# Optimization experiments

Hardware: AMD Instinct MI355X
Metric: run time of the kernel (lower is better)

## Reference

```python
import jax, jax.numpy as jnp
import numpy as np

N_ITERS = 21
TEMPERATURE = 0.04


def setup_inputs() -> dict:
    key = jax.random.key(0)
    input_tensor = jax.random.normal(key, (4096, 128, 128), dtype=jnp.float32)
    return {"input_tensor": input_tensor}


def reference(input_tensor) -> jnp.ndarray:
    n = input_tensor.shape[1]
    log_alpha = input_tensor.reshape((-1, n, n)) / TEMPERATURE

    def body(_, la):
        la = la - jax.nn.logsumexp(la, axis=2, keepdims=True)  # row normalize
        la = la - jax.nn.logsumexp(la, axis=1, keepdims=True)  # col normalize
        return la

    log_alpha = jax.lax.fori_loop(0, N_ITERS, body, log_alpha)
    return jnp.exp(log_alpha)
```

## Files before the change

### kernel.cpp

```cpp
#include <hip/hip_runtime.h>

typedef short bf16x8 __attribute__((ext_vector_type(8)));
typedef float f32x4 __attribute__((ext_vector_type(4)));
typedef unsigned int u32;
typedef unsigned short u16;

#define NIT 21
#define SMIN 1e-33f
#define LDSCOL 136

static __device__ __forceinline__ u16 f2bf(float f) {
    u32 u = __float_as_uint(f);
    u = (u + 0x7fffu + ((u >> 16) & 1u)) >> 16;
    return (u16)u;
}
static __device__ __forceinline__ float bf2f(u16 h) {
    return __uint_as_float(((u32)h) << 16);
}

__global__ __launch_bounds__(512)
void sinkhorn_kernel(const float* __restrict__ in, float* __restrict__ out) {
    const int t  = threadIdx.x;
    const int w  = t >> 6;
    const int lg = (t >> 4) & 3;
    const int ln = t & 15;
    const int M  = w * 16 + ln;
    const size_t mat = (size_t)blockIdx.x << 14;
    const float S = 36.067376022224085f;

    __shared__ __align__(16) u16 Ecm[128 * LDSCOL];
    __shared__ __align__(16) u16 a_lds[128];
    __shared__ __align__(16) u16 b_lds[128];

    bf16x8 af[4];

    {
        const float* src = in + mat + (size_t)M * 128 + lg * 8;
        float v[4][8];
        float m = -3.4e38f;
#pragma unroll
        for (int c = 0; c < 4; ++c) {
            float4 f0 = *(const float4*)(src + c * 32);
            float4 f1 = *(const float4*)(src + c * 32 + 4);
            v[c][0] = f0.x; v[c][1] = f0.y; v[c][2] = f0.z; v[c][3] = f0.w;
            v[c][4] = f1.x; v[c][5] = f1.y; v[c][6] = f1.z; v[c][7] = f1.w;
#pragma unroll
            for (int j = 0; j < 8; ++j) m = fmaxf(m, v[c][j]);
        }
        m = fmaxf(m, __shfl_xor(m, 16));
        m = fmaxf(m, __shfl_xor(m, 32));
        const float nms = -m * S;
        float s = 0.f;
#pragma unroll
        for (int c = 0; c < 4; ++c) {
            bf16x8 fr;
#pragma unroll
            for (int j = 0; j < 8; ++j) {
                float e = __builtin_amdgcn_exp2f(fmaf(v[c][j], S, nms));
                s += e;
                fr[j] = (short)f2bf(e);
            }
            af[c] = fr;
#pragma unroll
            for (int j = 0; j < 8; ++j)
                Ecm[(c * 32 + lg * 8 + j) * LDSCOL + M] = (u16)fr[j];
        }
        s += __shfl_xor(s, 16);
        s += __shfl_xor(s, 32);
        if (lg == 0) a_lds[M] = f2bf(__builtin_amdgcn_rcpf(fmaxf(s, SMIN)));
    }
    __syncthreads();

    const f32x4 z4 = {0.f, 0.f, 0.f, 0.f};

#pragma unroll 1
    for (int it = 0; it < NIT; ++it) {
        f32x4 acc = z4;
#pragma unroll
        for (int c = 0; c < 4; ++c) {
            const int kb = c * 32 + lg * 8;
            bf16x8 aop = *(const bf16x8*)&a_lds[kb];
            bf16x8 bop = *(const bf16x8*)&Ecm[M * LDSCOL + kb];
            acc = __builtin_amdgcn_mfma_f32_16x16x32_bf16(aop, bop, acc, 0, 0, 0);
        }
        if (lg == 0)
            b_lds[M] = f2bf(__builtin_amdgcn_rcpf(fmaxf(acc[0], SMIN)));
        __syncthreads();

        if (it < NIT - 1) {
            f32x4 r0 = z4;
#pragma unroll
            for (int c = 0; c < 4; ++c) {
                bf16x8 bop = *(const bf16x8*)&b_lds[c * 32 + lg * 8];
                r0 = __builtin_amdgcn_mfma_f32_16x16x32_bf16(af[c], bop, r0, 0, 0, 0);
            }
            if (ln == 0) {
#pragma unroll
                for (int r = 0; r < 4; ++r)
                    a_lds[w * 16 + lg * 4 + r] =
                        f2bf(__builtin_amdgcn_rcpf(fmaxf(r0[r], SMIN)));
            }
            __syncthreads();
        }
    }

    {
        float* dst = out + mat + (size_t)M * 128 + lg * 8;
        const float av = bf2f(a_lds[M]);
#pragma unroll
        for (int c = 0; c < 4; ++c) {
            const bf16x8 e = af[c];
            const bf16x8 bop = *(const bf16x8*)&b_lds[c * 32 + lg * 8];
            float4 o0, o1;
            o0.x = bf2f((u16)e[0]) * av * bf2f((u16)bop[0]);
            o0.y = bf2f((u16)e[1]) * av * bf2f((u16)bop[1]);
            o0.z = bf2f((u16)e[2]) * av * bf2f((u16)bop[2]);
            o0.w = bf2f((u16)e[3]) * av * bf2f((u16)bop[3]);
            o1.x = bf2f((u16)e[4]) * av * bf2f((u16)bop[4]);
            o1.y = bf2f((u16)e[5]) * av * bf2f((u16)bop[5]);
            o1.z = bf2f((u16)e[6]) * av * bf2f((u16)bop[6]);
            o1.w = bf2f((u16)e[7]) * av * bf2f((u16)bop[7]);
            *(float4*)(dst + c * 32)     = o0;
            *(float4*)(dst + c * 32 + 4) = o1;
        }
    }
}

extern "C" void kernel_launch(void* const* d_in, const int* in_sizes, int n_in,
                              void* d_out, int out_size, void* d_ws, size_t ws_size,
                              hipStream_t stream) {
    (void)n_in; (void)d_ws; (void)ws_size; (void)out_size;
    const float* in  = (const float*)d_in[0];
    float*       out = (float*)d_out;
    const int n_mat = in_sizes[0] / (128 * 128);
    sinkhorn_kernel<<<dim3(n_mat), dim3(512), 0, stream>>>(in, out);
}
```

Before: 150.5 us.

## Process two matrices per block to interleave independent MFMA chains

Each 512-thread block now handles two matrices instead of one, keeping two sets of LDS scaling vectors and exponent tiles and interleaving their MFMA chains within each Sinkhorn iteration. This halves the number of barriers per matrix and gives the scheduler independent MFMA work to hide latency in the serial row/column normalization loop. In exchange LDS use per block doubles (about 70 KB), which lowers occupancy, register pressure rises from holding two fragment sets, and the grid shrinks by half. An odd matrix count would leave the last matrix unprocessed.

```diff
diff --git a/kernel.cpp b/kernel.cpp
--- a/kernel.cpp
+++ b/kernel.cpp
@@ -25,17 +25,18 @@
     const int lg = (t >> 4) & 3;
     const int ln = t & 15;
     const int M  = w * 16 + ln;
-    const size_t mat = (size_t)blockIdx.x << 14;
+    const size_t mat0 = (size_t)(2 * blockIdx.x) << 14;
     const float S = 36.067376022224085f;
 
-    __shared__ __align__(16) u16 Ecm[128 * LDSCOL];
-    __shared__ __align__(16) u16 a_lds[128];
-    __shared__ __align__(16) u16 b_lds[128];
+    __shared__ __align__(16) u16 Ecm[2][128 * LDSCOL];
+    __shared__ __align__(16) u16 a_lds[2][128];
+    __shared__ __align__(16) u16 b_lds[2][128];
 
-    bf16x8 af[4];
+    bf16x8 af[2][4];
 
-    {
-        const float* src = in + mat + (size_t)M * 128 + lg * 8;
+#pragma unroll
+    for (int pm = 0; pm < 2; ++pm) {
+        const float* src = in + mat0 + ((size_t)pm << 14) + (size_t)M * 128 + lg * 8;
         float v[4][8];
         float m = -3.4e38f;
 #pragma unroll
@@ -60,14 +61,14 @@
                 s += e;
                 fr[j] = (short)f2bf(e);
             }
-            af[c] = fr;
+            af[pm][c] = fr;
 #pragma unroll
             for (int j = 0; j < 8; ++j)
-                Ecm[(c * 32 + lg * 8 + j) * LDSCOL + M] = (u16)fr[j];
+                Ecm[pm][(c * 32 + lg * 8 + j) * LDSCOL + M] = (u16)fr[j];
         }
         s += __shfl_xor(s, 16);
         s += __shfl_xor(s, 32);
-        if (lg == 0) a_lds[M] = f2bf(__builtin_amdgcn_rcpf(fmaxf(s, SMIN)));
+        if (lg == 0) a_lds[pm][M] = f2bf(__builtin_amdgcn_rcpf(fmaxf(s, SMIN)));
     }
     __syncthreads();
 
@@ -75,42 +76,54 @@
 
 #pragma unroll 1
     for (int it = 0; it < NIT; ++it) {
-        f32x4 acc = z4;
+        f32x4 acc0 = z4, acc1 = z4;
 #pragma unroll
         for (int c = 0; c < 4; ++c) {
             const int kb = c * 32 + lg * 8;
-            bf16x8 aop = *(const bf16x8*)&a_lds[kb];
-            bf16x8 bop = *(const bf16x8*)&Ecm[M * LDSCOL + kb];
-            acc = __builtin_amdgcn_mfma_f32_16x16x32_bf16(aop, bop, acc, 0, 0, 0);
+            bf16x8 a0 = *(const bf16x8*)&a_lds[0][kb];
+            bf16x8 e0 = *(const bf16x8*)&Ecm[0][M * LDSCOL + kb];
+            bf16x8 a1 = *(const bf16x8*)&a_lds[1][kb];
+            bf16x8 e1 = *(const bf16x8*)&Ecm[1][M * LDSCOL + kb];
+            acc0 = __builtin_amdgcn_mfma_f32_16x16x32_bf16(a0, e0, acc0, 0, 0, 0);
+            acc1 = __builtin_amdgcn_mfma_f32_16x16x32_bf16(a1, e1, acc1, 0, 0, 0);
         }
-        if (lg == 0)
-            b_lds[M] = f2bf(__builtin_amdgcn_rcpf(fmaxf(acc[0], SMIN)));
+        if (lg == 0) {
+            b_lds[0][M] = f2bf(__builtin_amdgcn_rcpf(fmaxf(acc0[0], SMIN)));
+            b_lds[1][M] = f2bf(__builtin_amdgcn_rcpf(fmaxf(acc1[0], SMIN)));
+        }
         __syncthreads();
 
         if (it < NIT - 1) {
-            f32x4 r0 = z4;
+            f32x4 r0 = z4, r1 = z4;
 #pragma unroll
             for (int c = 0; c < 4; ++c) {
-                bf16x8 bop = *(const bf16x8*)&b_lds[c * 32 + lg * 8];
-                r0 = __builtin_amdgcn_mfma_f32_16x16x32_bf16(af[c], bop, r0, 0, 0, 0);
+                const int kb = c * 32 + lg * 8;
+                bf16x8 b0 = *(const bf16x8*)&b_lds[0][kb];
+                bf16x8 b1 = *(const bf16x8*)&b_lds[1][kb];
+                r0 = __builtin_amdgcn_mfma_f32_16x16x32_bf16(af[0][c], b0, r0, 0, 0, 0);
+                r1 = __builtin_amdgcn_mfma_f32_16x16x32_bf16(af[1][c], b1, r1, 0, 0, 0);
             }
             if (ln == 0) {
 #pragma unroll
-                for (int r = 0; r < 4; ++r)
-                    a_lds[w * 16 + lg * 4 + r] =
+                for (int r = 0; r < 4; ++r) {
+                    a_lds[0][w * 16 + lg * 4 + r] =
                         f2bf(__builtin_amdgcn_rcpf(fmaxf(r0[r], SMIN)));
+                    a_lds[1][w * 16 + lg * 4 + r] =
+                        f2bf(__builtin_amdgcn_rcpf(fmaxf(r1[r], SMIN)));
+                }
             }
             __syncthreads();
         }
     }
 
-    {
-        float* dst = out + mat + (size_t)M * 128 + lg * 8;
-        const float av = bf2f(a_lds[M]);
+#pragma unroll
+    for (int pm = 0; pm < 2; ++pm) {
+        float* dst = out + mat0 + ((size_t)pm << 14) + (size_t)M * 128 + lg * 8;
+        const float av = bf2f(a_lds[pm][M]);
 #pragma unroll
         for (int c = 0; c < 4; ++c) {
-            const bf16x8 e = af[c];
-            const bf16x8 bop = *(const bf16x8*)&b_lds[c * 32 + lg * 8];
+            const bf16x8 e = af[pm][c];
+            const bf16x8 bop = *(const bf16x8*)&b_lds[pm][c * 32 + lg * 8];
             float4 o0, o1;
             o0.x = bf2f((u16)e[0]) * av * bf2f((u16)bop[0]);
             o0.y = bf2f((u16)e[1]) * av * bf2f((u16)bop[1]);
@@ -133,5 +146,5 @@
     const float* in  = (const float*)d_in[0];
     float*       out = (float*)d_out;
     const int n_mat = in_sizes[0] / (128 * 128);
-    sinkhorn_kernel<<<dim3(n_mat), dim3(512), 0, stream>>>(in, out);
+    sinkhorn_kernel<<<dim3(n_mat / 2), dim3(512), 0, stream>>>(in, out);
 }
```

New measurement: 251.9 us. 67.3% more time.

## Process each matrix with a single wavefront to eliminate block barriers

Applied to the files above, without the earlier changes.

Shrinks each block from 8 wavefronts to one, with that wave looping over all 8 row slabs and keeping all 32 bf16x8 fragments in registers. All __syncthreads calls go away, since the row and column scaling vectors are now produced and consumed within one wave. The trade-offs are much higher register pressure (af[8][4]), less latency hiding inside each block, and serial MFMA chains per wave. Occupancy now depends on LDS use per block (~35KB) and on how many single-wave blocks fit per CU.

```diff
diff --git a/kernel.cpp b/kernel.cpp
--- a/kernel.cpp
+++ b/kernel.cpp
@@ -18,13 +18,11 @@
     return __uint_as_float(((u32)h) << 16);
 }
 
-__global__ __launch_bounds__(512)
+__global__ __launch_bounds__(64, 1)
 void sinkhorn_kernel(const float* __restrict__ in, float* __restrict__ out) {
     const int t  = threadIdx.x;
-    const int w  = t >> 6;
     const int lg = (t >> 4) & 3;
     const int ln = t & 15;
-    const int M  = w * 16 + ln;
     const size_t mat = (size_t)blockIdx.x << 14;
     const float S = 36.067376022224085f;
 
@@ -32,9 +30,11 @@
     __shared__ __align__(16) u16 a_lds[128];
     __shared__ __align__(16) u16 b_lds[128];
 
-    bf16x8 af[4];
+    bf16x8 af[8][4];
 
-    {
+#pragma unroll
+    for (int s = 0; s < 8; ++s) {
+        const int M = s * 16 + ln;
         const float* src = in + mat + (size_t)M * 128 + lg * 8;
         float v[4][8];
         float m = -3.4e38f;
@@ -50,66 +50,76 @@
         m = fmaxf(m, __shfl_xor(m, 16));
         m = fmaxf(m, __shfl_xor(m, 32));
         const float nms = -m * S;
-        float s = 0.f;
+        float sum = 0.f;
 #pragma unroll
         for (int c = 0; c < 4; ++c) {
             bf16x8 fr;
 #pragma unroll
             for (int j = 0; j < 8; ++j) {
                 float e = __builtin_amdgcn_exp2f(fmaf(v[c][j], S, nms));
-                s += e;
+                sum += e;
                 fr[j] = (short)f2bf(e);
             }
-            af[c] = fr;
+            af[s][c] = fr;
 #pragma unroll
             for (int j = 0; j < 8; ++j)
                 Ecm[(c * 32 + lg * 8 + j) * LDSCOL + M] = (u16)fr[j];
         }
-        s += __shfl_xor(s, 16);
-        s += __shfl_xor(s, 32);
-        if (lg == 0) a_lds[M] = f2bf(__builtin_amdgcn_rcpf(fmaxf(s, SMIN)));
+        sum += __shfl_xor(sum, 16);
+        sum += __shfl_xor(sum, 32);
+        if (lg == 0) a_lds[M] = f2bf(__builtin_amdgcn_rcpf(fmaxf(sum, SMIN)));
     }
-    __syncthreads();
 
     const f32x4 z4 = {0.f, 0.f, 0.f, 0.f};
 
 #pragma unroll 1
     for (int it = 0; it < NIT; ++it) {
-        f32x4 acc = z4;
+        bf16x8 aop[4];
 #pragma unroll
-        for (int c = 0; c < 4; ++c) {
-            const int kb = c * 32 + lg * 8;
-            bf16x8 aop = *(const bf16x8*)&a_lds[kb];
-            bf16x8 bop = *(const bf16x8*)&Ecm[M * LDSCOL + kb];
-            acc = __builtin_amdgcn_mfma_f32_16x16x32_bf16(aop, bop, acc, 0, 0, 0);
+        for (int c = 0; c < 4; ++c)
+            aop[c] = *(const bf16x8*)&a_lds[c * 32 + lg * 8];
+#pragma unroll
+        for (int s = 0; s < 8; ++s) {
+            const int N = s * 16 + ln;
+            f32x4 acc = z4;
+#pragma unroll
+            for (int c = 0; c < 4; ++c) {
+                bf16x8 bop = *(const bf16x8*)&Ecm[N * LDSCOL + c * 32 + lg * 8];
+                acc = __builtin_amdgcn_mfma_f32_16x16x32_bf16(aop[c], bop, acc, 0, 0, 0);
+            }
+            if (lg == 0)
+                b_lds[N] = f2bf(__builtin_amdgcn_rcpf(fmaxf(acc[0], SMIN)));
         }
-        if (lg == 0)
-            b_lds[M] = f2bf(__builtin_amdgcn_rcpf(fmaxf(acc[0], SMIN)));
-        __syncthreads();
 
         if (it < NIT - 1) {
-            f32x4 r0 = z4;
+            bf16x8 bop[4];
 #pragma unroll
-            for (int c = 0; c < 4; ++c) {
-                bf16x8 bop = *(const bf16x8*)&b_lds[c * 32 + lg * 8];
-                r0 = __builtin_amdgcn_mfma_f32_16x16x32_bf16(af[c], bop, r0, 0, 0, 0);
+            for (int c = 0; c < 4; ++c)
+                bop[c] = *(const bf16x8*)&b_lds[c * 32 + lg * 8];
+#pragma unroll
+            for (int s = 0; s < 8; ++s) {
+                f32x4 r0 = z4;
+#pragma unroll
+                for (int c = 0; c < 4; ++c)
+                    r0 = __builtin_amdgcn_mfma_f32_16x16x32_bf16(af[s][c], bop[c], r0, 0, 0, 0);
+                if (ln == 0) {
+#pragma unroll
+                    for (int r = 0; r < 4; ++r)
+                        a_lds[s * 16 + lg * 4 + r] =
+                            f2bf(__builtin_amdgcn_rcpf(fmaxf(r0[r], SMIN)));
+                }
             }
-            if (ln == 0) {
-#pragma unroll
-                for (int r = 0; r < 4; ++r)
-                    a_lds[w * 16 + lg * 4 + r] =
-                        f2bf(__builtin_amdgcn_rcpf(fmaxf(r0[r], SMIN)));
-            }
-            __syncthreads();
         }
     }
 
-    {
+#pragma unroll
+    for (int s = 0; s < 8; ++s) {
+        const int M = s * 16 + ln;
         float* dst = out + mat + (size_t)M * 128 + lg * 8;
         const float av = bf2f(a_lds[M]);
 #pragma unroll
         for (int c = 0; c < 4; ++c) {
-            const bf16x8 e = af[c];
+            const bf16x8 e = af[s][c];
             const bf16x8 bop = *(const bf16x8*)&b_lds[c * 32 + lg * 8];
             float4 o0, o1;
             o0.x = bf2f((u16)e[0]) * av * bf2f((u16)bop[0]);
@@ -133,5 +143,5 @@
     const float* in  = (const float*)d_in[0];
     float*       out = (float*)d_out;
     const int n_mat = in_sizes[0] / (128 * 128);
-    sinkhorn_kernel<<<dim3(n_mat), dim3(512), 0, stream>>>(in, out);
+    sinkhorn_kernel<<<dim3(n_mat), dim3(64), 0, stream>>>(in, out);
 }
```

Measured after the change: 269.3 us. 1.79x slower.
